# Optimization experiments

Measured on AMD Instinct MI355X. Metric: run time of the kernel, lower is better.

The kernel has to match this reference:

```python
import jax, jax.numpy as jnp
import numpy as np

D_MODEL = 1024
N_HEADS = 16
D_K = D_MODEL // N_HEADS
B, T = 2, 2048


def setup_inputs() -> dict:
    key = jax.random.key(0)
    ks = jax.random.split(key, 9)
    s = 1.0 / np.sqrt(D_MODEL)
    def lin(kw, kb):
        W = jax.random.uniform(kw, (D_MODEL, D_MODEL), jnp.float32, -s, s)
        b = jax.random.uniform(kb, (D_MODEL,), jnp.float32, -s, s)
        return W, b
    Wq, bq = lin(ks[0], ks[1])
    Wk, bk = lin(ks[2], ks[3])
    Wv, bv = lin(ks[4], ks[5])
    Wo, bo = lin(ks[6], ks[7])
    x = jax.random.normal(ks[8], (B, T, D_MODEL), jnp.float32)
    return {"x": x, "Wq": Wq, "bq": bq, "Wk": Wk, "bk": bk,
            "Wv": Wv, "bv": bv, "Wo": Wo, "bo": bo}


def reference(x, Wq, bq, Wk, bk, Wv, bv, Wo, bo):
    Bn, Tn, _ = x.shape
    # torch Linear: x @ W.T + b
    def proj(W, b):
        y = x @ W.T + b  # [B, T, D]
        return y.reshape(Bn, Tn, N_HEADS, D_K).transpose(0, 2, 1, 3)  # [B, H, T, d_k]
    q = proj(Wq, bq)
    k = proj(Wk, bk)
    v = proj(Wv, bv)
    scores = jnp.einsum('bhqd,bhkd->bhqk', q, k) / jnp.sqrt(jnp.float32(D_K))
    causal = jnp.tril(jnp.ones((Tn, Tn), dtype=bool))  # True = keep
    scores = jnp.where(causal[None, None], scores, -jnp.inf)
    attn = jax.nn.softmax(scores, axis=-1)
    # dropout is identity in eval mode
    ctx = jnp.einsum('bhqk,bhkd->bhqd', attn, v)
    ctx = ctx.transpose(0, 2, 1, 3).reshape(Bn, Tn, D_MODEL)
    return ctx @ Wo.T + bo
```

## Files before the change

kernel.cpp:

```cpp
#include <hip/hip_runtime.h>
#include <hip/hip_bf16.h>
#include <stdint.h>

#define D_MODEL 1024
#define NH 16
#define DK 64
#define BB 2
#define TT 2048
#define NROWS (BB*TT)

typedef short bf16x8 __attribute__((ext_vector_type(8)));
typedef short bf16x4 __attribute__((ext_vector_type(4)));
typedef float f32x4  __attribute__((ext_vector_type(4)));

#if __has_builtin(__builtin_amdgcn_mfma_f32_16x16x16_bf16)
  #define MFMA16(a,b,c) __builtin_amdgcn_mfma_f32_16x16x16_bf16(a,b,c,0,0,0)
  #define HAVE_M16 1
#elif __has_builtin(__builtin_amdgcn_mfma_f32_16x16x16bf16_1k)
  #define MFMA16(a,b,c) __builtin_amdgcn_mfma_f32_16x16x16bf16_1k(a,b,c,0,0,0)
  #define HAVE_M16 1
#else
  #define HAVE_M16 0
#endif

#if __has_builtin(__builtin_amdgcn_global_load_lds)
  #define HAVE_GLDS 1
__device__ __forceinline__ void gload16(const unsigned short* g, unsigned short* lds){
    __builtin_amdgcn_global_load_lds(
        (const __attribute__((address_space(1))) unsigned int*)g,
        (__attribute__((address_space(3))) unsigned int*)lds, 16, 0, 0);
}
#else
  #define HAVE_GLDS 0
#endif

__device__ __forceinline__ unsigned pkbf(float a, float b){
    float2 t; t.x = a; t.y = b;
    __hip_bfloat162 h = __float22bfloat162_rn(t);
    return *reinterpret_cast<unsigned*>(&h);
}
__device__ __forceinline__ unsigned short bfbits(float a){
    __hip_bfloat16 h = __float2bfloat16(a);
    return *reinterpret_cast<unsigned short*>(&h);
}

__global__ __launch_bounds__(256) void conv_all(
    const float* __restrict__ x,
    const float* __restrict__ Wq, const float* __restrict__ Wk,
    const float* __restrict__ Wv, const float* __restrict__ Wo,
    unsigned short* __restrict__ xb, unsigned short* __restrict__ wb)
{
    const int blk = blockIdx.x;
    const float* src; unsigned short* dst; size_t i;
    if (blk < 2048) {
        src = x; dst = xb;
        i = ((size_t)blk * 256 + threadIdx.x) * 8;
    } else {
        const int t = (blk - 2048) >> 9;
        src = (t == 0) ? Wq : (t == 1) ? Wk : (t == 2) ? Wv : Wo;
        dst = wb + (size_t)t * D_MODEL * D_MODEL;
        i = ((size_t)((blk - 2048) & 511) * 256 + threadIdx.x) * 8;
    }
    float4 a = *(const float4*)(src + i);
    float4 b = *(const float4*)(src + i + 4);
    uint4 w;
    w.x = pkbf(a.x, a.y); w.y = pkbf(a.z, a.w);
    w.z = pkbf(b.x, b.y); w.w = pkbf(b.z, b.w);
    *(uint4*)(dst + i) = w;
}

__global__ __launch_bounds__(256) void conv_bf16(
    const float* __restrict__ x, unsigned short* __restrict__ y)
{
    size_t i = ((size_t)blockIdx.x * 256 + threadIdx.x) * 8;
    float4 a = *(const float4*)(x + i);
    float4 b = *(const float4*)(x + i + 4);
    uint4 w;
    w.x = pkbf(a.x, a.y); w.y = pkbf(a.z, a.w);
    w.z = pkbf(b.x, b.y); w.w = pkbf(b.z, b.w);
    *(uint4*)(y + i) = w;
}

#if HAVE_GLDS
template<int MI, int NB, bool CF32>
__device__ __forceinline__ void gemm_async(
    const unsigned short* __restrict__ Ap, const unsigned short* __restrict__ Bp,
    const float* __restrict__ bias, void* __restrict__ Cp,
    bool vt, float scale, unsigned short* As, unsigned short* Bs)
{
    constexpr int BMt = MI * 32, BNt = NB * 32;
    const int K = D_MODEL, N = D_MODEL;
    const int tid  = threadIdx.x;
    const int m0   = blockIdx.y * BMt;
    const int n0   = blockIdx.x * BNt;
    const int lane = tid & 63;
    const int w    = tid >> 6;
    const int wm   = (w >> 1) * (MI * 16);
    const int wn   = (w &  1) * (BNt / 2);
    const int l16  = lane & 15;
    const int quad = lane >> 4;
    const int crow = lane >> 2;
    const int ccol = (lane & 3) * 8;

    constexpr int CA = MI / 2;
    constexpr int CB = NB / 2;

    auto issue = [&](int buf, int k0){
        #pragma unroll
        for (int c = 0; c < CA; ++c) {
            const int chunk = w * CA + c;
            gload16(Ap + (size_t)(m0 + chunk*16 + crow) * K + k0 + ccol,
                    As + buf * BMt * 32 + chunk * 512);
        }
        #pragma unroll
        for (int c = 0; c < CB; ++c) {
            const int chunk = w * CB + c;
            gload16(Bp + (size_t)(n0 + chunk*16 + crow) * K + k0 + ccol,
                    Bs + buf * BNt * 32 + chunk * 512);
        }
    };

    f32x4 acc[MI][NB] = {};
    issue(0, 0);

    constexpr int ITER = D_MODEL / 32;
    for (int it = 0; it < ITER; ++it) {
        __syncthreads();
        if (it + 1 < ITER) issue((it + 1) & 1, (it + 1) * 32);
        const unsigned short* A = As + (it & 1) * BMt * 32;
        const unsigned short* B = Bs + (it & 1) * BNt * 32;
        bf16x8 af[MI], bg[NB];
        #pragma unroll
        for (int i = 0; i < MI; ++i)
            af[i] = *(const bf16x8*)&A[(wm + 16*i + l16) * 32 + quad * 8];
        #pragma unroll
        for (int j = 0; j < NB; ++j)
            bg[j] = *(const bf16x8*)&B[(wn + 16*j + l16) * 32 + quad * 8];
        #pragma unroll
        for (int i = 0; i < MI; ++i)
            #pragma unroll
            for (int j = 0; j < NB; ++j)
                acc[i][j] = __builtin_amdgcn_mfma_f32_16x16x32_bf16(af[i], bg[j], acc[i][j], 0, 0, 0);
    }

    #pragma unroll
    for (int j = 0; j < NB; ++j) {
        const int n = n0 + wn + 16*j + l16;
        const float bj = bias[n];
        #pragma unroll
        for (int i = 0; i < MI; ++i) {
            const int m = m0 + wm + 16*i + quad*4;
            if (vt) {
                const int b = m >> 11, t = m & 2047;
                ushort4 wv;
                wv.x = bfbits(acc[i][j][0] + bj);
                wv.y = bfbits(acc[i][j][1] + bj);
                wv.z = bfbits(acc[i][j][2] + bj);
                wv.w = bfbits(acc[i][j][3] + bj);
                *(ushort4*)((unsigned short*)Cp + (size_t)b * D_MODEL * TT
                            + (size_t)n * TT + t) = wv;
            } else {
                #pragma unroll
                for (int r = 0; r < 4; ++r) {
                    float v = (acc[i][j][r] + bj) * scale;
                    if (CF32) ((float*)Cp)[(size_t)(m + r) * N + n] = v;
                    else      ((__hip_bfloat16*)Cp)[(size_t)(m + r) * N + n] = __float2bfloat16(v);
                }
            }
        }
    }
}
#endif

#define ASTR 40

template<int MI, int NB, bool AF32, bool BF32, bool CF32>
__device__ __forceinline__ void gemm_body(
    const void* __restrict__ Ap, const void* __restrict__ Bp,
    const float* __restrict__ bias, void* __restrict__ Cp,
    bool vt, float scale, unsigned short* As, unsigned short* Bs)
{
    constexpr int BMt = MI * 32, BNt = NB * 32;
    const int K = D_MODEL, N = D_MODEL;
    const int tid  = threadIdx.x;
    const int m0   = blockIdx.y * BMt;
    const int n0   = blockIdx.x * BNt;
    const int lane = tid & 63;
    const int wave = tid >> 6;
    const int wm   = (wave >> 1) * (MI * 16);
    const int wn   = (wave &  1) * (BNt / 2);
    const int l16  = lane & 15;
    const int quad = lane >> 4;
    const int ar = (MI == 4) ? (tid >> 1) : (tid >> 2);
    const int ac = (MI == 4) ? ((tid & 1) * 16) : ((tid & 3) * 8);
    const int br = (NB == 4) ? (tid >> 1) : (tid >> 2);
    const int bc = (NB == 4) ? ((tid & 1) * 16) : ((tid & 3) * 8);

    uint4 pa[4], pb[4];

    auto loadA = [&](int k0){
        if (AF32) {
            const float* p = (const float*)Ap + (size_t)(m0 + ar) * K + k0 + ac;
            pa[0] = *(const uint4*)(p);     pa[1] = *(const uint4*)(p + 4);
            if (MI == 4) { pa[2] = *(const uint4*)(p + 8); pa[3] = *(const uint4*)(p + 12); }
        } else {
            const unsigned short* p = (const unsigned short*)Ap + (size_t)(m0 + ar) * K + k0 + ac;
            pa[0] = *(const uint4*)(p);
            if (MI == 4) pa[1] = *(const uint4*)(p + 8);
        }
    };
    auto loadB = [&](int k0){
        if (BF32) {
            const float* p = (const float*)Bp + (size_t)(n0 + br) * K + k0 + bc;
            pb[0] = *(const uint4*)(p); pb[1] = *(const uint4*)(p + 4);
            if (NB == 4) { pb[2] = *(const uint4*)(p + 8); pb[3] = *(const uint4*)(p + 12); }
        } else {
            const unsigned short* p = (const unsigned short*)Bp + (size_t)(n0 + br) * K + k0 + bc;
            pb[0] = *(const uint4*)(p);
            if (NB == 4) pb[1] = *(const uint4*)(p + 8);
        }
    };
    auto stage = [&](int buf){
        unsigned short* A = As + buf * BMt * ASTR;
        unsigned short* B = Bs + buf * BNt * ASTR;
        if (AF32) {
            const float* f = (const float*)pa;
            uint4 w0;
            w0.x = pkbf(f[0], f[1]); w0.y = pkbf(f[2], f[3]);
            w0.z = pkbf(f[4], f[5]); w0.w = pkbf(f[6], f[7]);
            *(uint4*)&A[ar*ASTR + ac] = w0;
            if (MI == 4) {
                uint4 w1;
                w1.x = pkbf(f[8], f[9]);   w1.y = pkbf(f[10], f[11]);
                w1.z = pkbf(f[12], f[13]); w1.w = pkbf(f[14], f[15]);
                *(uint4*)&A[ar*ASTR + ac + 8] = w1;
            }
        } else {
            *(uint4*)&A[ar*ASTR + ac] = pa[0];
            if (MI == 4) *(uint4*)&A[ar*ASTR + ac + 8] = pa[1];
        }
        if (BF32) {
            const float* g = (const float*)pb;
            uint4 v0;
            v0.x = pkbf(g[0], g[1]); v0.y = pkbf(g[2], g[3]);
            v0.z = pkbf(g[4], g[5]); v0.w = pkbf(g[6], g[7]);
            *(uint4*)&B[br*ASTR + bc] = v0;
            if (NB == 4) {
                uint4 v1;
                v1.x = pkbf(g[8], g[9]);   v1.y = pkbf(g[10], g[11]);
                v1.z = pkbf(g[12], g[13]); v1.w = pkbf(g[14], g[15]);
                *(uint4*)&B[br*ASTR + bc + 8] = v1;
            }
        } else {
            *(uint4*)&B[br*ASTR + bc] = pb[0];
            if (NB == 4) *(uint4*)&B[br*ASTR + bc + 8] = pb[1];
        }
    };

    f32x4 acc[MI][NB] = {};
    loadA(0); loadB(0);
    stage(0);

    constexpr int ITER = D_MODEL / 32;
    for (int it = 0; it < ITER; ++it) {
        __syncthreads();
        if (it + 1 < ITER) { loadA((it + 1) * 32); loadB((it + 1) * 32); }
        const unsigned short* A = As + (it & 1) * BMt * ASTR;
        const unsigned short* B = Bs + (it & 1) * BNt * ASTR;
        bf16x8 af[MI], bg[NB];
        #pragma unroll
        for (int i = 0; i < MI; ++i)
            af[i] = *(const bf16x8*)&A[(wm + 16*i + l16) * ASTR + quad * 8];
        #pragma unroll
        for (int j = 0; j < NB; ++j)
            bg[j] = *(const bf16x8*)&B[(wn + 16*j + l16) * ASTR + quad * 8];
        #pragma unroll
        for (int i = 0; i < MI; ++i)
            #pragma unroll
            for (int j = 0; j < NB; ++j)
                acc[i][j] = __builtin_amdgcn_mfma_f32_16x16x32_bf16(af[i], bg[j], acc[i][j], 0, 0, 0);
        if (it + 1 < ITER) stage((it + 1) & 1);
    }

    #pragma unroll
    for (int j = 0; j < NB; ++j) {
        const int n = n0 + wn + 16*j + l16;
        const float bj = bias[n];
        #pragma unroll
        for (int i = 0; i < MI; ++i) {
            const int m = m0 + wm + 16*i + quad*4;
            if (vt) {
                const int b = m >> 11, t = m & 2047;
                ushort4 wv;
                wv.x = bfbits(acc[i][j][0] + bj);
                wv.y = bfbits(acc[i][j][1] + bj);
                wv.z = bfbits(acc[i][j][2] + bj);
                wv.w = bfbits(acc[i][j][3] + bj);
                *(ushort4*)((unsigned short*)Cp + (size_t)b * D_MODEL * TT
                            + (size_t)n * TT + t) = wv;
            } else {
                #pragma unroll
                for (int r = 0; r < 4; ++r) {
                    float v = (acc[i][j][r] + bj) * scale;
                    if (CF32) ((float*)Cp)[(size_t)(m + r) * N + n] = v;
                    else      ((__hip_bfloat16*)Cp)[(size_t)(m + r) * N + n] = __float2bfloat16(v);
                }
            }
        }
    }
}

template<bool AF32, bool BF32>
__device__ __forceinline__ void qkv_sel(
    const void* x,
    const void* Wq, const float* bq, const void* Wk, const float* bk,
    const void* Wv, const float* bv,
    __hip_bfloat16* Qw, __hip_bfloat16* Kd, __hip_bfloat16* Vd,
    unsigned short* As, unsigned short* Bs)
{
    const void* W; const float* bi; void* C; bool vt = false; float sc = 1.0f;
    if      (blockIdx.z == 0) { W = Wq; bi = bq; C = Qw; sc = 0.125f; }
    else if (blockIdx.z == 1) { W = Wk; bi = bk; C = Kd; }
    else                      { W = Wv; bi = bv; C = Vd; vt = true; }
    gemm_body<4, 4, AF32, BF32, false>(x, W, bi, C, vt, sc, As, Bs);
}

#define QKV_KERNEL(name, AF, BF, XT)                                          \
__global__ __launch_bounds__(256, 3) void name(                               \
    const XT* __restrict__ x,                                                 \
    const void* __restrict__ Wq, const float* __restrict__ bq,                \
    const void* __restrict__ Wk, const float* __restrict__ bk,                \
    const void* __restrict__ Wv, const float* __restrict__ bv,                \
    __hip_bfloat16* __restrict__ Qw, __hip_bfloat16* __restrict__ Kd,         \
    __hip_bfloat16* __restrict__ Vd)                                          \
{                                                                             \
    __shared__ __align__(16) unsigned short As[2*128*ASTR];                   \
    __shared__ __align__(16) unsigned short Bs[2*128*ASTR];                   \
    qkv_sel<AF, BF>(x, Wq, bq, Wk, bk, Wv, bv, Qw, Kd, Vd, As, Bs);           \
}
QKV_KERNEL(gemm_qkv_f32, true,  true,  float)
QKV_KERNEL(gemm_qkv_xb,  false, true,  unsigned short)

__global__ __launch_bounds__(256, 3) void gemm_qkv_bb(
    const unsigned short* __restrict__ x,
    const unsigned short* __restrict__ Wq, const float* __restrict__ bq,
    const unsigned short* __restrict__ Wk, const float* __restrict__ bk,
    const unsigned short* __restrict__ Wv, const float* __restrict__ bv,
    __hip_bfloat16* __restrict__ Qw, __hip_bfloat16* __restrict__ Kd,
    __hip_bfloat16* __restrict__ Vd)
{
#if HAVE_GLDS
    __shared__ __align__(16) unsigned short As[2*128*32];
    __shared__ __align__(16) unsigned short Bs[2*128*32];
    const unsigned short* W; const float* bi; void* C; bool vt = false; float sc = 1.0f;
    if      (blockIdx.z == 0) { W = Wq; bi = bq; C = Qw; sc = 0.125f; }
    else if (blockIdx.z == 1) { W = Wk; bi = bk; C = Kd; }
    else                      { W = Wv; bi = bv; C = Vd; vt = true; }
    gemm_async<4, 4, false>(x, W, bi, C, vt, sc, As, Bs);
#else
    __shared__ __align__(16) unsigned short As[2*128*ASTR];
    __shared__ __align__(16) unsigned short Bs[2*128*ASTR];
    qkv_sel<false, false>(x, Wq, bq, Wk, bk, Wv, bv, Qw, Kd, Vd, As, Bs);
#endif
}

__global__ __launch_bounds__(256, 2) void gemm_out_f(
    const __hip_bfloat16* __restrict__ ctx, const void* __restrict__ Wo,
    const float* __restrict__ bo, float* __restrict__ out)
{
    __shared__ __align__(16) unsigned short As[2*128*ASTR];
    __shared__ __align__(16) unsigned short Bs[2*64*ASTR];
    gemm_body<4, 2, false, true, true>(ctx, Wo, bo, out, false, 1.0f, As, Bs);
}

__global__ __launch_bounds__(256, 2) void gemm_out_b(
    const __hip_bfloat16* __restrict__ ctx, const unsigned short* __restrict__ Wo,
    const float* __restrict__ bo, float* __restrict__ out)
{
#if HAVE_GLDS
    __shared__ __align__(16) unsigned short As[2*128*32];
    __shared__ __align__(16) unsigned short Bs[2*64*32];
    gemm_async<4, 2, true>((const unsigned short*)ctx, Wo, bo, out, false, 1.0f, As, Bs);
#else
    __shared__ __align__(16) unsigned short As[2*128*ASTR];
    __shared__ __align__(16) unsigned short Bs[2*64*ASTR];
    gemm_body<4, 2, false, false, true>(ctx, Wo, bo, out, false, 1.0f, As, Bs);
#endif
}

#define QSTR 68

__global__ __launch_bounds__(256, 3) void attn_mfma(
    const __hip_bfloat16* __restrict__ Q,
    const __hip_bfloat16* __restrict__ Km,
    const __hip_bfloat16* __restrict__ Vt,
    __hip_bfloat16* __restrict__ ctx)
{
    __shared__ __align__(16) unsigned short Ks [2][64*QSTR];
    __shared__ __align__(16) unsigned short VTs[2][64*QSTR];
    __shared__ __align__(16) unsigned short QP [64*QSTR];

    const int tid = threadIdx.x;
    const int blk = blockIdx.x;
    const int qt  = 31 - (blk & 31);
    const int h   = (blk >> 5) & 15;
    const int b   = blk >> 9;
    const int q0  = qt << 6;
    const size_t rowbase = (size_t)b * TT;
    const int colbase = h * DK;

    const int lane = tid & 63;
    const int w    = tid >> 6;
    const int l16  = lane & 15;
    const int quad = lane >> 4;
    const int lr = tid >> 2;
    const int lc = (tid & 3) << 4;

    const unsigned short* Vtb = (const unsigned short*)Vt + (size_t)b * D_MODEL * TT;

    uint4 kr0, kr1, vt0, vt1;
    auto prefetch = [&](int kv0){
        const unsigned short* pk = (const unsigned short*)Km +
            (rowbase + kv0 + lr) * D_MODEL + colbase + lc;
        kr0 = *(const uint4*)(pk);
        kr1 = *(const uint4*)(pk + 8);
        const unsigned short* pv = Vtb + (size_t)(colbase + lr) * TT + kv0 + lc;
        vt0 = *(const uint4*)(pv);
        vt1 = *(const uint4*)(pv + 8);
    };
    auto stageKV = [&](int buf){
        *(uint4*)&Ks [buf][lr*QSTR + lc]     = kr0;
        *(uint4*)&Ks [buf][lr*QSTR + lc + 8] = kr1;
        *(uint4*)&VTs[buf][lr*QSTR + lc]     = vt0;
        *(uint4*)&VTs[buf][lr*QSTR + lc + 8] = vt1;
    };

    {
        const unsigned short* p = (const unsigned short*)Q +
            (rowbase + q0 + lr) * D_MODEL + colbase + lc;
        *(uint4*)&QP[lr*QSTR + lc]     = *(const uint4*)(p);
        *(uint4*)&QP[lr*QSTR + lc + 8] = *(const uint4*)(p + 8);
    }
    prefetch(0);
    __syncthreads();
    bf16x8 af_q0 = *(const bf16x8*)&QP[(16*w + l16)*QSTR + quad*8];
    bf16x8 af_q1 = *(const bf16x8*)&QP[(16*w + l16)*QSTR + quad*8 + 32];
    stageKV(0);

#if HAVE_M16
    f32x4 o[4] = {};
    float lpart = 0.0f;

    for (int kt = 0; kt <= qt; ++kt) {
        __syncthreads();
        if (kt < qt) prefetch((kt + 1) << 6);
        const int cur = kt & 1;
        const bool diag = (kt == qt);

        f32x4 s[4] = {};
        #pragma unroll
        for (int cb = 0; cb < 4; ++cb) {
            bf16x8 ak0 = *(const bf16x8*)&Ks[cur][(16*cb + l16)*QSTR + quad*8];
            bf16x8 ak1 = *(const bf16x8*)&Ks[cur][(16*cb + l16)*QSTR + quad*8 + 32];
            s[cb] = __builtin_amdgcn_mfma_f32_16x16x32_bf16(ak0, af_q0, s[cb], 0, 0, 0);
            s[cb] = __builtin_amdgcn_mfma_f32_16x16x32_bf16(ak1, af_q1, s[cb], 0, 0, 0);
        }

        bf16x4 bp[4];
        #pragma unroll
        for (int cb = 0; cb < 4; ++cb) {
            float p[4];
            #pragma unroll
            for (int r = 0; r < 4; ++r) {
                float v = fminf(s[cb][r], 25.0f);
                bool keep = !diag || (16*cb + quad*4 + r <= 16*w + l16);
                p[r] = keep ? __expf(v) : 0.0f;
                lpart += p[r];
            }
            uint2 u; u.x = pkbf(p[0], p[1]); u.y = pkbf(p[2], p[3]);
            bp[cb] = *reinterpret_cast<bf16x4*>(&u);
        }

        #pragma unroll
        for (int nb = 0; nb < 4; ++nb)
            #pragma unroll
            for (int cb = 0; cb < 4; ++cb) {
                bf16x4 av = *(const bf16x4*)&VTs[cur][(16*nb + l16)*QSTR + 16*cb + quad*4];
                o[nb] = MFMA16(av, bp[cb], o[nb]);
            }

        if (kt < qt) stageKV((kt + 1) & 1);
    }

    lpart += __shfl_xor(lpart, 16);
    lpart += __shfl_xor(lpart, 32);
    const float inv_l = 1.0f / lpart;

    {
        const size_t row = (rowbase + q0 + 16*w + l16) * (size_t)D_MODEL + colbase;
        #pragma unroll
        for (int nb = 0; nb < 4; ++nb) {
            ushort4 wv;
            wv.x = bfbits(o[nb][0] * inv_l);
            wv.y = bfbits(o[nb][1] * inv_l);
            wv.z = bfbits(o[nb][2] * inv_l);
            wv.w = bfbits(o[nb][3] * inv_l);
            *(ushort4*)((unsigned short*)ctx + row + 16*nb + quad*4) = wv;
        }
    }
#else
    const short ob = (short)0x3F80;
    bf16x8 ones = { ob, ob, ob, ob, ob, ob, ob, ob };
    f32x4 o[4] = {};
    f32x4 l_acc = {};

    for (int kt = 0; kt <= qt; ++kt) {
        __syncthreads();
        if (kt < qt) prefetch((kt + 1) << 6);
        const int cur = kt & 1;

        f32x4 s[4] = {};
        #pragma unroll
        for (int cb = 0; cb < 4; ++cb) {
            bf16x8 bk0 = *(const bf16x8*)&Ks[cur][(16*cb + l16)*QSTR + quad*8];
            bf16x8 bk1 = *(const bf16x8*)&Ks[cur][(16*cb + l16)*QSTR + quad*8 + 32];
            s[cb] = __builtin_amdgcn_mfma_f32_16x16x32_bf16(af_q0, bk0, s[cb], 0, 0, 0);
            s[cb] = __builtin_amdgcn_mfma_f32_16x16x32_bf16(af_q1, bk1, s[cb], 0, 0, 0);
        }
        const bool diag = (kt == qt);
        #pragma unroll
        for (int cb = 0; cb < 4; ++cb)
            #pragma unroll
            for (int r = 0; r < 4; ++r) {
                float v = fminf(s[cb][r], 25.0f);
                float p = (diag && (16*cb + l16 > 16*w + quad*4 + r)) ? 0.0f : __expf(v);
                QP[(16*w + quad*4 + r)*QSTR + 16*cb + l16] = bfbits(p);
            }
        bf16x8 ap0 = *(const bf16x8*)&QP[(16*w + l16)*QSTR + quad*8];
        bf16x8 ap1 = *(const bf16x8*)&QP[(16*w + l16)*QSTR + quad*8 + 32];
        #pragma unroll
        for (int nb = 0; nb < 4; ++nb) {
            bf16x8 bv0 = *(const bf16x8*)&VTs[cur][(16*nb + l16)*QSTR + quad*8];
            bf16x8 bv1 = *(const bf16x8*)&VTs[cur][(16*nb + l16)*QSTR + quad*8 + 32];
            o[nb] = __builtin_amdgcn_mfma_f32_16x16x32_bf16(ap0, bv0, o[nb], 0, 0, 0);
            o[nb] = __builtin_amdgcn_mfma_f32_16x16x32_bf16(ap1, bv1, o[nb], 0, 0, 0);
        }
        l_acc = __builtin_amdgcn_mfma_f32_16x16x32_bf16(ap0, ones, l_acc, 0, 0, 0);
        l_acc = __builtin_amdgcn_mfma_f32_16x16x32_bf16(ap1, ones, l_acc, 0, 0, 0);
        if (kt < qt) stageKV((kt + 1) & 1);
    }
    float inv_l[4];
    #pragma unroll
    for (int r = 0; r < 4; ++r) inv_l[r] = 1.0f / l_acc[r];
    #pragma unroll
    for (int nb = 0; nb < 4; ++nb)
        #pragma unroll
        for (int r = 0; r < 4; ++r) {
            const int row = q0 + 16*w + quad*4 + r;
            ctx[(rowbase + row)*D_MODEL + colbase + 16*nb + l16] =
                __float2bfloat16(o[nb][r] * inv_l[r]);
        }
#endif
}

extern "C" void kernel_launch(void* const* d_in, const int* in_sizes, int n_in,
                              void* d_out, int out_size, void* d_ws, size_t ws_size,
                              hipStream_t stream) {
    const float* x  = (const float*)d_in[0];
    const float* Wq = (const float*)d_in[1];
    const float* bq = (const float*)d_in[2];
    const float* Wk = (const float*)d_in[3];
    const float* bk = (const float*)d_in[4];
    const float* Wv = (const float*)d_in[5];
    const float* bv = (const float*)d_in[6];
    const float* Wo = (const float*)d_in[7];
    const float* bo = (const float*)d_in[8];

    __hip_bfloat16* Qw = (__hip_bfloat16*)d_ws;
    __hip_bfloat16* Kd = (__hip_bfloat16*)d_out;
    __hip_bfloat16* Vd = Kd + (size_t)NROWS * D_MODEL;
    unsigned short* xb = (unsigned short*)d_ws + (size_t)NROWS * D_MODEL;
    unsigned short* wb = xb + (size_t)NROWS * D_MODEL;
    const size_t WSZ = (size_t)D_MODEL * D_MODEL;

    dim3 gqkv(D_MODEL / 128, NROWS / 128, 3);
    dim3 gout(D_MODEL / 64, NROWS / 128);
    const bool haveXB = ws_size >= (size_t)(16u << 20);
    const bool haveWB = ws_size >= (size_t)(24u << 20);

    if (haveWB) {
        conv_all<<<4096, 256, 0, stream>>>(x, Wq, Wk, Wv, Wo, xb, wb);
        gemm_qkv_bb<<<gqkv, 256, 0, stream>>>(xb, wb, bq, wb + WSZ, bk,
                                              wb + 2*WSZ, bv, Qw, Kd, Vd);
    } else if (haveXB) {
        conv_bf16<<<(NROWS * D_MODEL) / (256 * 8), 256, 0, stream>>>(x, xb);
        gemm_qkv_xb<<<gqkv, 256, 0, stream>>>(xb, Wq, bq, Wk, bk, Wv, bv, Qw, Kd, Vd);
    } else {
        gemm_qkv_f32<<<gqkv, 256, 0, stream>>>(x, Wq, bq, Wk, bk, Wv, bv, Qw, Kd, Vd);
    }

    attn_mfma<<<BB * NH * (TT / 64), 256, 0, stream>>>(Qw, Kd, Vd, Qw);

    if (haveWB)
        gemm_out_b<<<gout, 256, 0, stream>>>(Qw, wb + 3*WSZ, bo, (float*)d_out);
    else
        gemm_out_f<<<gout, 256, 0, stream>>>(Qw, Wo, bo, (float*)d_out);
}
```

Measured before the change: 202.6 us.

## Rebalance causal attention with paired query tiles, exp2 softmax, and deeper out-proj K staging

Rewrites the attention kernel as single-wave blocks, each handling a pair of 16-row query tiles (one low, one high) so that causal work is balanced per block. Work is mapped to XCDs so heads share K/V in cache, and KV is staged in 32-key chunks. Softmax now uses exp2 with log2(e) folded into the Q scale, and s_setprio is placed around the MFMA sections. The output projection GEMM stages two K-slices per sync, doubling its LDS use, and the old fallback path without 16x16x16 MFMA is removed.

Result: slower. 254.9 us (+25.8%).

```diff
diff --git a/kernel.cpp b/kernel.cpp
--- a/kernel.cpp
+++ b/kernel.cpp
@@ -9,18 +9,18 @@
 #define TT 2048
 #define NROWS (BB*TT)
 
+#define QSCALE 0.180336880f
+
 typedef short bf16x8 __attribute__((ext_vector_type(8)));
 typedef short bf16x4 __attribute__((ext_vector_type(4)));
 typedef float f32x4  __attribute__((ext_vector_type(4)));
 
 #if __has_builtin(__builtin_amdgcn_mfma_f32_16x16x16_bf16)
   #define MFMA16(a,b,c) __builtin_amdgcn_mfma_f32_16x16x16_bf16(a,b,c,0,0,0)
-  #define HAVE_M16 1
 #elif __has_builtin(__builtin_amdgcn_mfma_f32_16x16x16bf16_1k)
   #define MFMA16(a,b,c) __builtin_amdgcn_mfma_f32_16x16x16bf16_1k(a,b,c,0,0,0)
-  #define HAVE_M16 1
 #else
-  #define HAVE_M16 0
+  #define MFMA16(a,b,c) (c)
 #endif
 
 #if __has_builtin(__builtin_amdgcn_global_load_lds)
@@ -33,6 +33,14 @@
 #else
   #define HAVE_GLDS 0
 #endif
+
+__device__ __forceinline__ float fexp2(float x){
+#if __has_builtin(__builtin_amdgcn_exp2f)
+    return __builtin_amdgcn_exp2f(x);
+#else
+    return exp2f(x);
+#endif
+}
 
 __device__ __forceinline__ unsigned pkbf(float a, float b){
     float2 t; t.x = a; t.y = b;
@@ -82,7 +90,7 @@
 }
 
 #if HAVE_GLDS
-template<int MI, int NB, bool CF32>
+template<int MI, int NB, bool CF32, int KU>
 __device__ __forceinline__ void gemm_async(
     const unsigned short* __restrict__ Ap, const unsigned short* __restrict__ Bp,
     const float* __restrict__ bias, void* __restrict__ Cp,
@@ -105,42 +113,48 @@
     constexpr int CA = MI / 2;
     constexpr int CB = NB / 2;
 
-    auto issue = [&](int buf, int k0){
-        #pragma unroll
-        for (int c = 0; c < CA; ++c) {
-            const int chunk = w * CA + c;
-            gload16(Ap + (size_t)(m0 + chunk*16 + crow) * K + k0 + ccol,
-                    As + buf * BMt * 32 + chunk * 512);
-        }
-        #pragma unroll
-        for (int c = 0; c < CB; ++c) {
-            const int chunk = w * CB + c;
-            gload16(Bp + (size_t)(n0 + chunk*16 + crow) * K + k0 + ccol,
-                    Bs + buf * BNt * 32 + chunk * 512);
+    auto issue = [&](int grp, int k0){
+        #pragma unroll
+        for (int u = 0; u < KU; ++u) {
+            #pragma unroll
+            for (int c = 0; c < CA; ++c) {
+                const int chunk = w * CA + c;
+                gload16(Ap + (size_t)(m0 + chunk*16 + crow) * K + k0 + u*32 + ccol,
+                        As + (grp*KU + u) * BMt * 32 + chunk * 512);
+            }
+            #pragma unroll
+            for (int c = 0; c < CB; ++c) {
+                const int chunk = w * CB + c;
+                gload16(Bp + (size_t)(n0 + chunk*16 + crow) * K + k0 + u*32 + ccol,
+                        Bs + (grp*KU + u) * BNt * 32 + chunk * 512);
+            }
         }
     };
 
     f32x4 acc[MI][NB] = {};
     issue(0, 0);
 
-    constexpr int ITER = D_MODEL / 32;
-    for (int it = 0; it < ITER; ++it) {
+    constexpr int NG = D_MODEL / (32 * KU);
+    for (int g = 0; g < NG; ++g) {
         __syncthreads();
-        if (it + 1 < ITER) issue((it + 1) & 1, (it + 1) * 32);
-        const unsigned short* A = As + (it & 1) * BMt * 32;
-        const unsigned short* B = Bs + (it & 1) * BNt * 32;
-        bf16x8 af[MI], bg[NB];
-        #pragma unroll
-        for (int i = 0; i < MI; ++i)
-            af[i] = *(const bf16x8*)&A[(wm + 16*i + l16) * 32 + quad * 8];
-        #pragma unroll
-        for (int j = 0; j < NB; ++j)
-            bg[j] = *(const bf16x8*)&B[(wn + 16*j + l16) * 32 + quad * 8];
-        #pragma unroll
-        for (int i = 0; i < MI; ++i)
+        if (g + 1 < NG) issue((g + 1) & 1, (g + 1) * (32 * KU));
+        #pragma unroll
+        for (int u = 0; u < KU; ++u) {
+            const unsigned short* A = As + ((g & 1) * KU + u) * BMt * 32;
+            const unsigned short* B = Bs + ((g & 1) * KU + u) * BNt * 32;
+            bf16x8 af[MI], bg[NB];
+            #pragma unroll
+            for (int i = 0; i < MI; ++i)
+                af[i] = *(const bf16x8*)&A[(wm + 16*i + l16) * 32 + quad * 8];
             #pragma unroll
             for (int j = 0; j < NB; ++j)
-                acc[i][j] = __builtin_amdgcn_mfma_f32_16x16x32_bf16(af[i], bg[j], acc[i][j], 0, 0, 0);
+                bg[j] = *(const bf16x8*)&B[(wn + 16*j + l16) * 32 + quad * 8];
+            #pragma unroll
+            for (int i = 0; i < MI; ++i)
+                #pragma unroll
+                for (int j = 0; j < NB; ++j)
+                    acc[i][j] = __builtin_amdgcn_mfma_f32_16x16x32_bf16(af[i], bg[j], acc[i][j], 0, 0, 0);
+        }
     }
 
     #pragma unroll
@@ -319,7 +333,7 @@
     unsigned short* As, unsigned short* Bs)
 {
     const void* W; const float* bi; void* C; bool vt = false; float sc = 1.0f;
-    if      (blockIdx.z == 0) { W = Wq; bi = bq; C = Qw; sc = 0.125f; }
+    if      (blockIdx.z == 0) { W = Wq; bi = bq; C = Qw; sc = QSCALE; }
     else if (blockIdx.z == 1) { W = Wk; bi = bk; C = Kd; }
     else                      { W = Wv; bi = bv; C = Vd; vt = true; }
     gemm_body<4, 4, AF32, BF32, false>(x, W, bi, C, vt, sc, As, Bs);
@@ -353,10 +367,10 @@
     __shared__ __align__(16) unsigned short As[2*128*32];
     __shared__ __align__(16) unsigned short Bs[2*128*32];
     const unsigned short* W; const float* bi; void* C; bool vt = false; float sc = 1.0f;
-    if      (blockIdx.z == 0) { W = Wq; bi = bq; C = Qw; sc = 0.125f; }
+    if      (blockIdx.z == 0) { W = Wq; bi = bq; C = Qw; sc = QSCALE; }
     else if (blockIdx.z == 1) { W = Wk; bi = bk; C = Kd; }
     else                      { W = Wv; bi = bv; C = Vd; vt = true; }
-    gemm_async<4, 4, false>(x, W, bi, C, vt, sc, As, Bs);
+    gemm_async<4, 4, false, 1>(x, W, bi, C, vt, sc, As, Bs);
 #else
     __shared__ __align__(16) unsigned short As[2*128*ASTR];
     __shared__ __align__(16) unsigned short Bs[2*128*ASTR];
@@ -378,9 +392,9 @@
     const float* __restrict__ bo, float* __restrict__ out)
 {
 #if HAVE_GLDS
-    __shared__ __align__(16) unsigned short As[2*128*32];
-    __shared__ __align__(16) unsigned short Bs[2*64*32];
-    gemm_async<4, 2, true>((const unsigned short*)ctx, Wo, bo, out, false, 1.0f, As, Bs);
+    __shared__ __align__(16) unsigned short As[2*2*128*32];
+    __shared__ __align__(16) unsigned short Bs[2*2*64*32];
+    gemm_async<4, 2, true, 2>((const unsigned short*)ctx, Wo, bo, out, false, 1.0f, As, Bs);
 #else
     __shared__ __align__(16) unsigned short As[2*128*ASTR];
     __shared__ __align__(16) unsigned short Bs[2*64*ASTR];
@@ -388,116 +402,140 @@
 #endif
 }
 
-#define QSTR 68
-
-__global__ __launch_bounds__(256, 3) void attn_mfma(
+#define KSTR 68
+#define VSTR 36
+
+__global__ __launch_bounds__(64, 2) void attn_mfma(
     const __hip_bfloat16* __restrict__ Q,
     const __hip_bfloat16* __restrict__ Km,
     const __hip_bfloat16* __restrict__ Vt,
     __hip_bfloat16* __restrict__ ctx)
 {
-    __shared__ __align__(16) unsigned short Ks [2][64*QSTR];
-    __shared__ __align__(16) unsigned short VTs[2][64*QSTR];
-    __shared__ __align__(16) unsigned short QP [64*QSTR];
+    __shared__ __align__(16) unsigned short Ks[2][32*KSTR];
+    __shared__ __align__(16) unsigned short Vs[2][64*VSTR];
 
     const int tid = threadIdx.x;
-    const int blk = blockIdx.x;
-    const int qt  = 31 - (blk & 31);
-    const int h   = (blk >> 5) & 15;
-    const int b   = blk >> 9;
-    const int q0  = qt << 6;
+    const int id  = blockIdx.x;
+    const int xcd = id & 7;
+    const int r   = id >> 3;
+    const int sub = r & 3;
+    const int pr  = r >> 2;
+    const int qq  = pr & 7, kk = pr >> 3;
+    const int p   = (kk & 1) ? (67 - qq - 4*kk) : (qq + 4*kk);
+    const int bh  = xcd * 4 + sub;
+    const int b   = bh >> 4, h = bh & 15;
+    const int tl  = p, th = 127 - p;
+    const int slow = tl >> 1;
+    const int send = th >> 1;
     const size_t rowbase = (size_t)b * TT;
     const int colbase = h * DK;
 
-    const int lane = tid & 63;
-    const int w    = tid >> 6;
-    const int l16  = lane & 15;
-    const int quad = lane >> 4;
-    const int lr = tid >> 2;
-    const int lc = (tid & 3) << 4;
+    const int l16 = tid & 15, quad = tid >> 4;
 
     const unsigned short* Vtb = (const unsigned short*)Vt + (size_t)b * D_MODEL * TT;
 
-    uint4 kr0, kr1, vt0, vt1;
-    auto prefetch = [&](int kv0){
+    uint4 kp0, kp1, kp2, kp3, vp0, vp1, vp2, vp3;
+    auto prefetch = [&](int st){
+        const int kv0 = st << 5;
         const unsigned short* pk = (const unsigned short*)Km +
-            (rowbase + kv0 + lr) * D_MODEL + colbase + lc;
-        kr0 = *(const uint4*)(pk);
-        kr1 = *(const uint4*)(pk + 8);
-        const unsigned short* pv = Vtb + (size_t)(colbase + lr) * TT + kv0 + lc;
-        vt0 = *(const uint4*)(pv);
-        vt1 = *(const uint4*)(pv + 8);
-    };
-    auto stageKV = [&](int buf){
-        *(uint4*)&Ks [buf][lr*QSTR + lc]     = kr0;
-        *(uint4*)&Ks [buf][lr*QSTR + lc + 8] = kr1;
-        *(uint4*)&VTs[buf][lr*QSTR + lc]     = vt0;
-        *(uint4*)&VTs[buf][lr*QSTR + lc + 8] = vt1;
-    };
-
-    {
-        const unsigned short* p = (const unsigned short*)Q +
-            (rowbase + q0 + lr) * D_MODEL + colbase + lc;
-        *(uint4*)&QP[lr*QSTR + lc]     = *(const uint4*)(p);
-        *(uint4*)&QP[lr*QSTR + lc + 8] = *(const uint4*)(p + 8);
-    }
+            (rowbase + kv0 + (tid >> 1)) * D_MODEL + colbase + (tid & 1) * 32;
+        kp0 = *(const uint4*)(pk);      kp1 = *(const uint4*)(pk + 8);
+        kp2 = *(const uint4*)(pk + 16); kp3 = *(const uint4*)(pk + 24);
+        const unsigned short* pv = Vtb + (size_t)(colbase + tid) * TT + kv0;
+        vp0 = *(const uint4*)(pv);      vp1 = *(const uint4*)(pv + 8);
+        vp2 = *(const uint4*)(pv + 16); vp3 = *(const uint4*)(pv + 24);
+    };
+    auto stage = [&](int buf){
+        unsigned short* kd = &Ks[buf][(tid >> 1) * KSTR + (tid & 1) * 32];
+        *(uint4*)(kd)      = kp0; *(uint4*)(kd + 8)  = kp1;
+        *(uint4*)(kd + 16) = kp2; *(uint4*)(kd + 24) = kp3;
+        unsigned short* vd = &Vs[buf][tid * VSTR];
+        *(uint4*)(vd)      = vp0; *(uint4*)(vd + 8)  = vp1;
+        *(uint4*)(vd + 16) = vp2; *(uint4*)(vd + 24) = vp3;
+    };
+
+    const unsigned short* qpl = (const unsigned short*)Q +
+        (rowbase + tl*16 + l16) * D_MODEL + colbase + quad*8;
+    bf16x8 aql0 = *(const bf16x8*)(qpl);
+    bf16x8 aql1 = *(const bf16x8*)(qpl + 32);
+    const unsigned short* qph = (const unsigned short*)Q +
+        (rowbase + th*16 + l16) * D_MODEL + colbase + quad*8;
+    bf16x8 aqh0 = *(const bf16x8*)(qph);
+    bf16x8 aqh1 = *(const bf16x8*)(qph + 32);
+
     prefetch(0);
-    __syncthreads();
-    bf16x8 af_q0 = *(const bf16x8*)&QP[(16*w + l16)*QSTR + quad*8];
-    bf16x8 af_q1 = *(const bf16x8*)&QP[(16*w + l16)*QSTR + quad*8 + 32];
-    stageKV(0);
-
-#if HAVE_M16
-    f32x4 o[4] = {};
-    float lpart = 0.0f;
-
-    for (int kt = 0; kt <= qt; ++kt) {
+    stage(0);
+
+    f32x4 ol[4] = {}, oh[4] = {};
+    float lpl = 0.0f, lph = 0.0f;
+
+    auto dounit = [&](const bf16x8* ak0, const bf16x8* ak1, const bf16x4 (*av)[2],
+                      bf16x8 aq0, bf16x8 aq1, f32x4* o, float& lp,
+                      bool diag, int par){
+        f32x4 sa[2] = {};
+        __builtin_amdgcn_s_setprio(1);
+        #pragma unroll
+        for (int cb = 0; cb < 2; ++cb) {
+            sa[cb] = __builtin_amdgcn_mfma_f32_16x16x32_bf16(ak0[cb], aq0, sa[cb], 0, 0, 0);
+            sa[cb] = __builtin_amdgcn_mfma_f32_16x16x32_bf16(ak1[cb], aq1, sa[cb], 0, 0, 0);
+        }
+        __builtin_amdgcn_s_setprio(0);
+        bf16x4 bp[2];
+        #pragma unroll
+        for (int cb = 0; cb < 2; ++cb) {
+            float pv4[4];
+            #pragma unroll
+            for (int rr = 0; rr < 4; ++rr) {
+                float v = fminf(sa[cb][rr], 36.0f);
+                bool keep = !diag || (16*cb + quad*4 + rr <= (par << 4) + l16);
+                pv4[rr] = keep ? fexp2(v) : 0.0f;
+                lp += pv4[rr];
+            }
+            uint2 u; u.x = pkbf(pv4[0], pv4[1]); u.y = pkbf(pv4[2], pv4[3]);
+            bp[cb] = *reinterpret_cast<bf16x4*>(&u);
+        }
+        __builtin_amdgcn_s_setprio(1);
+        #pragma unroll
+        for (int nb = 0; nb < 4; ++nb)
+            #pragma unroll
+            for (int cb = 0; cb < 2; ++cb)
+                o[nb] = MFMA16(av[nb][cb], bp[cb], o[nb]);
+        __builtin_amdgcn_s_setprio(0);
+    };
+
+    for (int s = 0; s <= send; ++s) {
         __syncthreads();
-        if (kt < qt) prefetch((kt + 1) << 6);
-        const int cur = kt & 1;
-        const bool diag = (kt == qt);
-
-        f32x4 s[4] = {};
-        #pragma unroll
-        for (int cb = 0; cb < 4; ++cb) {
-            bf16x8 ak0 = *(const bf16x8*)&Ks[cur][(16*cb + l16)*QSTR + quad*8];
-            bf16x8 ak1 = *(const bf16x8*)&Ks[cur][(16*cb + l16)*QSTR + quad*8 + 32];
-            s[cb] = __builtin_amdgcn_mfma_f32_16x16x32_bf16(ak0, af_q0, s[cb], 0, 0, 0);
-            s[cb] = __builtin_amdgcn_mfma_f32_16x16x32_bf16(ak1, af_q1, s[cb], 0, 0, 0);
-        }
-
-        bf16x4 bp[4];
-        #pragma unroll
-        for (int cb = 0; cb < 4; ++cb) {
-            float p[4];
-            #pragma unroll
-            for (int r = 0; r < 4; ++r) {
-                float v = fminf(s[cb][r], 25.0f);
-                bool keep = !diag || (16*cb + quad*4 + r <= 16*w + l16);
-                p[r] = keep ? __expf(v) : 0.0f;
-                lpart += p[r];
-            }
-            uint2 u; u.x = pkbf(p[0], p[1]); u.y = pkbf(p[2], p[3]);
-            bp[cb] = *reinterpret_cast<bf16x4*>(&u);
-        }
-
+        if (s < send) prefetch(s + 1);
+        const int cur = s & 1;
+
+        bf16x8 ak0[2], ak1[2];
+        #pragma unroll
+        for (int cb = 0; cb < 2; ++cb) {
+            ak0[cb] = *(const bf16x8*)&Ks[cur][(16*cb + l16)*KSTR + quad*8];
+            ak1[cb] = *(const bf16x8*)&Ks[cur][(16*cb + l16)*KSTR + quad*8 + 32];
+        }
+        bf16x4 av[4][2];
         #pragma unroll
         for (int nb = 0; nb < 4; ++nb)
             #pragma unroll
-            for (int cb = 0; cb < 4; ++cb) {
-                bf16x4 av = *(const bf16x4*)&VTs[cur][(16*nb + l16)*QSTR + 16*cb + quad*4];
-                o[nb] = MFMA16(av, bp[cb], o[nb]);
-            }
-
-        if (kt < qt) stageKV((kt + 1) & 1);
-    }
-
-    lpart += __shfl_xor(lpart, 16);
-    lpart += __shfl_xor(lpart, 32);
-    const float inv_l = 1.0f / lpart;
-
-    {
-        const size_t row = (rowbase + q0 + 16*w + l16) * (size_t)D_MODEL + colbase;
+            for (int cb = 0; cb < 2; ++cb)
+                av[nb][cb] = *(const bf16x4*)&Vs[cur][(16*nb + l16)*VSTR + 16*cb + quad*4];
+
+        if (s <= slow) {
+            if (s == slow) dounit(ak0, ak1, av, aql0, aql1, ol, lpl, true,  tl & 1);
+            else           dounit(ak0, ak1, av, aql0, aql1, ol, lpl, false, 0);
+        }
+        if (s == send)     dounit(ak0, ak1, av, aqh0, aqh1, oh, lph, true,  th & 1);
+        else               dounit(ak0, ak1, av, aqh0, aqh1, oh, lph, false, 0);
+
+        if (s < send) stage((s + 1) & 1);
+    }
+
+    auto finish = [&](const f32x4* o, float lp, int trow){
+        lp += __shfl_xor(lp, 16);
+        lp += __shfl_xor(lp, 32);
+        const float inv_l = 1.0f / lp;
+        const size_t row = (rowbase + trow + l16) * (size_t)D_MODEL + colbase;
         #pragma unroll
         for (int nb = 0; nb < 4; ++nb) {
             ushort4 wv;
@@ -507,60 +545,9 @@
             wv.w = bfbits(o[nb][3] * inv_l);
             *(ushort4*)((unsigned short*)ctx + row + 16*nb + quad*4) = wv;
         }
-    }
-#else
-    const short ob = (short)0x3F80;
-    bf16x8 ones = { ob, ob, ob, ob, ob, ob, ob, ob };
-    f32x4 o[4] = {};
-    f32x4 l_acc = {};
-
-    for (int kt = 0; kt <= qt; ++kt) {
-        __syncthreads();
-        if (kt < qt) prefetch((kt + 1) << 6);
-        const int cur = kt & 1;
-
-        f32x4 s[4] = {};
-        #pragma unroll
-        for (int cb = 0; cb < 4; ++cb) {
-            bf16x8 bk0 = *(const bf16x8*)&Ks[cur][(16*cb + l16)*QSTR + quad*8];
-            bf16x8 bk1 = *(const bf16x8*)&Ks[cur][(16*cb + l16)*QSTR + quad*8 + 32];
-            s[cb] = __builtin_amdgcn_mfma_f32_16x16x32_bf16(af_q0, bk0, s[cb], 0, 0, 0);
-            s[cb] = __builtin_amdgcn_mfma_f32_16x16x32_bf16(af_q1, bk1, s[cb], 0, 0, 0);
-        }
-        const bool diag = (kt == qt);
-        #pragma unroll
-        for (int cb = 0; cb < 4; ++cb)
-            #pragma unroll
-            for (int r = 0; r < 4; ++r) {
-                float v = fminf(s[cb][r], 25.0f);
-                float p = (diag && (16*cb + l16 > 16*w + quad*4 + r)) ? 0.0f : __expf(v);
-                QP[(16*w + quad*4 + r)*QSTR + 16*cb + l16] = bfbits(p);
-            }
-        bf16x8 ap0 = *(const bf16x8*)&QP[(16*w + l16)*QSTR + quad*8];
-        bf16x8 ap1 = *(const bf16x8*)&QP[(16*w + l16)*QSTR + quad*8 + 32];
-        #pragma unroll
-        for (int nb = 0; nb < 4; ++nb) {
-            bf16x8 bv0 = *(const bf16x8*)&VTs[cur][(16*nb + l16)*QSTR + quad*8];
-            bf16x8 bv1 = *(const bf16x8*)&VTs[cur][(16*nb + l16)*QSTR + quad*8 + 32];
-            o[nb] = __builtin_amdgcn_mfma_f32_16x16x32_bf16(ap0, bv0, o[nb], 0, 0, 0);
-            o[nb] = __builtin_amdgcn_mfma_f32_16x16x32_bf16(ap1, bv1, o[nb], 0, 0, 0);
-        }
-        l_acc = __builtin_amdgcn_mfma_f32_16x16x32_bf16(ap0, ones, l_acc, 0, 0, 0);
-        l_acc = __builtin_amdgcn_mfma_f32_16x16x32_bf16(ap1, ones, l_acc, 0, 0, 0);
-        if (kt < qt) stageKV((kt + 1) & 1);
-    }
-    float inv_l[4];
-    #pragma unroll
-    for (int r = 0; r < 4; ++r) inv_l[r] = 1.0f / l_acc[r];
-    #pragma unroll
-    for (int nb = 0; nb < 4; ++nb)
-        #pragma unroll
-        for (int r = 0; r < 4; ++r) {
-            const int row = q0 + 16*w + quad*4 + r;
-            ctx[(rowbase + row)*D_MODEL + colbase + 16*nb + l16] =
-                __float2bfloat16(o[nb][r] * inv_l[r]);
-        }
-#endif
+    };
+    finish(ol, lpl, tl * 16);
+    finish(oh, lph, th * 16);
 }
 
 extern "C" void kernel_launch(void* const* d_in, const int* in_sizes, int n_in,
@@ -599,7 +586,7 @@
         gemm_qkv_f32<<<gqkv, 256, 0, stream>>>(x, Wq, bq, Wk, bk, Wv, bv, Qw, Kd, Vd);
     }
 
-    attn_mfma<<<BB * NH * (TT / 64), 256, 0, stream>>>(Qw, Kd, Vd, Qw);
+    attn_mfma<<<2048, 64, 0, stream>>>(Qw, Kd, Vd, Qw);
 
     if (haveWB)
         gemm_out_b<<<gout, 256, 0, stream>>>(Qw, wb + 3*WSZ, bo, (float*)d_out);
```
